# Kernel tuning notes

Measured on AMD Instinct MI355X. Metric: run time of the kernel, lower is better.

## Reference

```python
import jax, jax.numpy as jnp
import numpy as np

B, P, T = 4096, 16, 8
IN_DIM, OUT_DIM, K = 128, 128, 2
N_TABLE = 100000


def setup_inputs() -> dict:
    key = jax.random.key(0)
    ks = jax.random.split(key, 8)
    return {
        "path_input": jax.random.randint(ks[0], (B, P, T), 0, N_TABLE, dtype=jnp.int32),
        "path_num": P,
        "timestamp": T,
        "path_type": jax.random.randint(ks[1], (T,), 0, 4, dtype=jnp.int32),
        "user_emb": jax.random.normal(ks[2], (N_TABLE, IN_DIM), jnp.float32),
        "item_emb": jax.random.normal(ks[3], (N_TABLE, IN_DIM), jnp.float32),
        "ca_emb": jax.random.normal(ks[4], (N_TABLE, IN_DIM), jnp.float32),
        "ci_emb": jax.random.normal(ks[5], (N_TABLE, IN_DIM), jnp.float32),
        "conv_w": jax.random.normal(ks[6], (OUT_DIM, IN_DIM, K), jnp.float32) * 0.05,
        "conv_b": jax.random.normal(ks[7], (OUT_DIM,), jnp.float32) * 0.05,
    }


def reference(path_input, path_num, timestamp, path_type,
              user_emb, item_emb, ca_emb, ci_emb, conv_w, conv_b):
    b, p, t = path_input.shape
    # [4, N, D] stacked tables; per-position table selection via path_type
    tables = jnp.stack([user_emb, item_emb, ca_emb, ci_emb])
    # emb: [B, P, T, D]  (advanced indexing: path_type broadcasts over B, P)
    emb = tables[path_type[None, None, :], path_input]
    # conv1d over time: [B*P, D, T] -> [B*P, out, T-K+1]
    x = emb.reshape(b * p, t, -1).transpose(0, 2, 1)
    y = jax.lax.conv_general_dilated(
        x, conv_w, window_strides=(1,), padding='VALID',
        dimension_numbers=('NCH', 'OIH', 'NCH')) + conv_b[None, :, None]
    # max-pool over time, then over paths (dropout is identity in eval)
    y = y.max(axis=-1).reshape(b, p, -1)  # [B, P, out]
    return y.max(axis=1)  # [B, out]
```

## Files before the change

### kernel.cpp

```cpp
#include <hip/hip_runtime.h>

#define NB   4096
#define NBLK 256
#define NJ   16

typedef __attribute__((ext_vector_type(4))) float f32x4;
typedef __attribute__((ext_vector_type(8))) short short8;
typedef __attribute__((ext_vector_type(4))) int   int4v;

union Frag { int4v i; short8 s; };

__device__ __forceinline__ unsigned short f2bf(float f) {
  unsigned int u = __float_as_uint(f);
  u = (u + 0x7FFFu + ((u >> 16) & 1u)) >> 16;
  return (unsigned short)u;
}

__device__ __forceinline__ int cvtpk(float lo, float hi) {
  int r;
  asm("v_cvt_pk_bf16_f32 %0, %1, %2" : "=v"(r) : "v"(lo), "v"(hi));
  return r;
}

__global__ __launch_bounds__(512)
void wconv_kernel(const float* __restrict__ conv_w, unsigned short* __restrict__ ws)
{
  int flat = blockIdx.x * 512 + threadIdx.x;
  int lane = flat & 63;
  int ng   = (flat >> 6) & 7;
  int ker  = (flat >> 9) & 1;
  int kk   = flat >> 10;
  int col  = ng * 16 + (lane & 15);
  int k0   = kk * 32 + (lane >> 4) * 8;
  short8 s;
#pragma unroll
  for (int j = 0; j < 8; ++j)
    s[j] = (short)f2bf(conv_w[col * 256 + (k0 + j) * 2 + ker]);
  *(short8*)(ws + (size_t)flat * 8) = s;
}

#define A0_OFF  0
#define A1_OFF  34816
#define RED_OFF 69632
#define IDX_OFF 86016
#define PTR_OFF 94208
#define LDS_BYTES 94272
#define A_STRIDE 272

__global__ __launch_bounds__(512, 2)
void path_emb_kernel(const int* __restrict__ path_input,
                     const int* __restrict__ path_type,
                     const float* __restrict__ t0, const float* __restrict__ t1,
                     const float* __restrict__ t2, const float* __restrict__ t3,
                     const unsigned short* __restrict__ wfrag,
                     const float* __restrict__ conv_b,
                     float* __restrict__ out)
{
  __shared__ __align__(16) char lds[LDS_BYTES];
  const int blk  = blockIdx.x;
  const int tid  = threadIdx.x;
  const int wid  = tid >> 6;
  const int lane = tid & 63;
  const int lrow = lane & 15;
  const int lk   = lane >> 4;
  const int R = wid & 1;
  const int C = wid >> 1;

  ((int4v*)(lds + IDX_OFF))[tid] =
      ((const int4v*)(path_input + (size_t)blk * NJ * 128))[tid];
  if (tid < 8) {
    int ty = path_type[tid];
    const float* tb = (ty == 0) ? t0 : (ty == 1) ? t1 : (ty == 2) ? t2 : t3;
    ((const float**)(lds + PTR_OFF))[tid] = tb;
  }

  Frag wreg[4][2][2];
#pragma unroll
  for (int kk = 0; kk < 4; ++kk)
#pragma unroll
    for (int ker = 0; ker < 2; ++ker)
#pragma unroll
      for (int n = 0; n < 2; ++n) {
        int f = (kk * 2 + ker) * 8 + C * 2 + n;
        wreg[kk][ker][n].i = *(const int4v*)(wfrag + (size_t)f * 512 + lane * 8);
      }
  __syncthreads();

  const int grow = tid >> 2;
  const int gq   = tid & 3;

  auto ISSUE = [&](int j, f32x4 (&ld)[8]) {
    int idx = ((const int*)(lds + IDX_OFF))[j * 128 + grow];
    const float* tb = ((const float* const*)(lds + PTR_OFF))[grow & 7];
    const float* g  = tb + (size_t)idx * 128 + gq * 32;
#pragma unroll
    for (int i = 0; i < 8; ++i) ld[i] = *(const f32x4*)(g + i * 4);
  };
  auto WRITE = [&](int bufoff, const f32x4 (&ld)[8]) {
    char* dst = lds + bufoff + grow * A_STRIDE + gq * 64;
#pragma unroll
    for (int i = 0; i < 4; ++i) {
      int4v w;
      w[0] = cvtpk(ld[2 * i][0], ld[2 * i][1]);
      w[1] = cvtpk(ld[2 * i][2], ld[2 * i][3]);
      w[2] = cvtpk(ld[2 * i + 1][0], ld[2 * i + 1][1]);
      w[3] = cvtpk(ld[2 * i + 1][2], ld[2 * i + 1][3]);
      *(int4v*)(dst + i * 16) = w;
    }
  };

  {
    f32x4 ld0[8];
    ISSUE(0, ld0);
    WRITE(A0_OFF, ld0);
  }
  __syncthreads();

  float* red = (float*)(lds + RED_OFF);
  const int arow0 = R * 64 + lrow;

  for (int j = 0; j < NJ; ++j) {
    const int bufc = (j & 1) ? A1_OFF : A0_OFF;
    const int bufn = (j & 1) ? A0_OFF : A1_OFF;
    const bool pf  = (j + 1 < NJ);

    f32x4 ld[8];
    if (pf) ISSUE(j + 1, ld);
    __builtin_amdgcn_sched_barrier(0);

    f32x4 accA[4][2] = {};
    f32x4 accB[4][2] = {};
    const char* Ab = lds + bufc;
#pragma unroll
    for (int kk = 0; kk < 4; ++kk) {
      Frag a[4];
#pragma unroll
      for (int m = 0; m < 4; ++m)
        a[m].i = *(const int4v*)(Ab + (arow0 + m * 16) * A_STRIDE + kk * 64 + lk * 16);
#pragma unroll
      for (int m = 0; m < 4; ++m)
#pragma unroll
        for (int n = 0; n < 2; ++n) {
          accA[m][n] = __builtin_amdgcn_mfma_f32_16x16x32_bf16(
              a[m].s, wreg[kk][0][n].s, accA[m][n], 0, 0, 0);
          accB[m][n] = __builtin_amdgcn_mfma_f32_16x16x32_bf16(
              a[m].s, wreg[kk][1][n].s, accB[m][n], 0, 0, 0);
        }
    }

    float vmax[2] = {-1e30f, -1e30f};
#pragma unroll
    for (int m = 0; m < 4; ++m)
#pragma unroll
      for (int n = 0; n < 2; ++n) {
        float up = __shfl_down(accB[m][n][0], 16);
#pragma unroll
        for (int r = 0; r < 4; ++r) {
          int rloc = lk * 4 + r;
          if ((rloc & 7) == 7) continue;
          float y2 = (r < 3) ? accB[m][n][r + 1] : up;
          vmax[n] = fmaxf(vmax[n], accA[m][n][r] + y2);
        }
      }
#pragma unroll
    for (int n = 0; n < 2; ++n) {
      float v = vmax[n];
      v = fmaxf(v, __shfl_xor(v, 16));
      v = fmaxf(v, __shfl_xor(v, 32));
      vmax[n] = v;
    }
    if (lane < 16) {
#pragma unroll
      for (int n = 0; n < 2; ++n)
        red[R * (NJ * 128) + j * 128 + C * 32 + n * 16 + lane] = vmax[n];
    }

    if (pf) WRITE(bufn, ld);
    __syncthreads();
  }

  {
    const int j  = tid >> 5;
    const int c0 = (tid & 31) * 4;
    const float* redA = (const float*)(lds + RED_OFF);
    const float* redB = redA + NJ * 128;
    f32x4 va = *(const f32x4*)(redA + j * 128 + c0);
    f32x4 vb = *(const f32x4*)(redB + j * 128 + c0);
    f32x4 bb = *(const f32x4*)(conv_b + c0);
    f32x4 o;
#pragma unroll
    for (int k = 0; k < 4; ++k) o[k] = fmaxf(va[k], vb[k]) + bb[k];
    *(f32x4*)(out + (size_t)(blk * NJ + j) * 128 + c0) = o;
  }
}

extern "C" void kernel_launch(void* const* d_in, const int* in_sizes, int n_in,
                              void* d_out, int out_size, void* d_ws, size_t ws_size,
                              hipStream_t stream) {
  const int*   path_input = (const int*)d_in[0];
  const int*   path_type  = (const int*)d_in[3];
  const float* user_emb   = (const float*)d_in[4];
  const float* item_emb   = (const float*)d_in[5];
  const float* ca_emb     = (const float*)d_in[6];
  const float* ci_emb     = (const float*)d_in[7];
  const float* conv_w     = (const float*)d_in[8];
  const float* conv_b     = (const float*)d_in[9];
  float* out = (float*)d_out;
  unsigned short* wfrag = (unsigned short*)d_ws;

  wconv_kernel<<<dim3(8), dim3(512), 0, stream>>>(conv_w, wfrag);
  path_emb_kernel<<<dim3(NBLK), dim3(512), 0, stream>>>(
      path_input, path_type, user_emb, item_emb, ca_emb, ci_emb,
      wfrag, conv_b, out);
}
```

Before: 52.54 us.

## Deepen gather prefetch to two stages and interleave per-thread row chunks

The embedding gather now keeps two register sets in flight, so loads for step j+2 are issued while step j is computed. This hides more global latency than the old single-step prefetch. Each thread's gather now reads interleaved 16-byte chunks (stride 64 bytes) instead of one contiguous 128-byte span, and writes 8-byte LDS stores instead of 16-byte ones. The __syncthreads is replaced by a manual lgkmcnt wait plus s_barrier. The cost is extra register pressure from two load buffers, which matters under launch_bounds(512,2). The narrower LDS stores may also add bank conflicts.

```diff
diff --git a/kernel.cpp b/kernel.cpp
--- a/kernel.cpp
+++ b/kernel.cpp
@@ -7,6 +7,7 @@
 typedef __attribute__((ext_vector_type(4))) float f32x4;
 typedef __attribute__((ext_vector_type(8))) short short8;
 typedef __attribute__((ext_vector_type(4))) int   int4v;
+typedef __attribute__((ext_vector_type(2))) int   int2v;
 
 union Frag { int4v i; short8 s; };
 
@@ -92,42 +93,25 @@
   auto ISSUE = [&](int j, f32x4 (&ld)[8]) {
     int idx = ((const int*)(lds + IDX_OFF))[j * 128 + grow];
     const float* tb = ((const float* const*)(lds + PTR_OFF))[grow & 7];
-    const float* g  = tb + (size_t)idx * 128 + gq * 32;
-#pragma unroll
-    for (int i = 0; i < 8; ++i) ld[i] = *(const f32x4*)(g + i * 4);
+    const float* g  = tb + (size_t)idx * 128 + gq * 4;
+#pragma unroll
+    for (int i = 0; i < 8; ++i) ld[i] = *(const f32x4*)(g + i * 16);
   };
   auto WRITE = [&](int bufoff, const f32x4 (&ld)[8]) {
-    char* dst = lds + bufoff + grow * A_STRIDE + gq * 64;
-#pragma unroll
-    for (int i = 0; i < 4; ++i) {
-      int4v w;
-      w[0] = cvtpk(ld[2 * i][0], ld[2 * i][1]);
-      w[1] = cvtpk(ld[2 * i][2], ld[2 * i][3]);
-      w[2] = cvtpk(ld[2 * i + 1][0], ld[2 * i + 1][1]);
-      w[3] = cvtpk(ld[2 * i + 1][2], ld[2 * i + 1][3]);
-      *(int4v*)(dst + i * 16) = w;
-    }
-  };
-
-  {
-    f32x4 ld0[8];
-    ISSUE(0, ld0);
-    WRITE(A0_OFF, ld0);
-  }
-  __syncthreads();
+    char* dst = lds + bufoff + grow * A_STRIDE + gq * 8;
+#pragma unroll
+    for (int i = 0; i < 8; ++i) {
+      int2v w;
+      w[0] = cvtpk(ld[i][0], ld[i][1]);
+      w[1] = cvtpk(ld[i][2], ld[i][3]);
+      *(int2v*)(dst + i * 32) = w;
+    }
+  };
 
   float* red = (float*)(lds + RED_OFF);
   const int arow0 = R * 64 + lrow;
 
-  for (int j = 0; j < NJ; ++j) {
-    const int bufc = (j & 1) ? A1_OFF : A0_OFF;
-    const int bufn = (j & 1) ? A0_OFF : A1_OFF;
-    const bool pf  = (j + 1 < NJ);
-
-    f32x4 ld[8];
-    if (pf) ISSUE(j + 1, ld);
-    __builtin_amdgcn_sched_barrier(0);
-
+  auto COMPUTE = [&](int bufc, int j) {
     f32x4 accA[4][2] = {};
     f32x4 accB[4][2] = {};
     const char* Ab = lds + bufc;
@@ -147,7 +131,6 @@
               a[m].s, wreg[kk][1][n].s, accB[m][n], 0, 0, 0);
         }
     }
-
     float vmax[2] = {-1e30f, -1e30f};
 #pragma unroll
     for (int m = 0; m < 4; ++m)
@@ -174,9 +157,33 @@
       for (int n = 0; n < 2; ++n)
         red[R * (NJ * 128) + j * 128 + C * 32 + n * 16 + lane] = vmax[n];
     }
-
-    if (pf) WRITE(bufn, ld);
-    __syncthreads();
+  };
+
+  auto BAR = [&]() {
+    asm volatile("s_waitcnt lgkmcnt(0)" ::: "memory");
+    __builtin_amdgcn_sched_barrier(0);
+    __builtin_amdgcn_s_barrier();
+    __builtin_amdgcn_sched_barrier(0);
+  };
+
+  f32x4 ldA[8], ldB[8];
+  ISSUE(0, ldA);
+  WRITE(A0_OFF, ldA);
+  ISSUE(1, ldB);
+  BAR();
+
+#pragma unroll 1
+  for (int j = 0; j < NJ; j += 2) {
+    if (j + 2 < NJ) ISSUE(j + 2, ldA);
+    __builtin_amdgcn_sched_barrier(0);
+    COMPUTE(A0_OFF, j);
+    WRITE(A1_OFF, ldB);
+    BAR();
+    if (j + 3 < NJ) ISSUE(j + 3, ldB);
+    __builtin_amdgcn_sched_barrier(0);
+    COMPUTE(A1_OFF, j + 1);
+    if (j + 2 < NJ) WRITE(A0_OFF, ldA);
+    BAR();
   }
 
   {
```

New measurement: 51.96 us. Within noise of the previous version (-1.1%).
